# Kernel optimization log

Measured on AMD Instinct MI355X. Metric: run time of the kernel, lower is better.

The kernel has to match this reference:

```python
import jax, jax.numpy as jnp
import numpy as np

B, S, D = 2, 2048, 1024
H, DC = 16, 16          # num_heads, head_coord_dim
CD = 16                 # coord_dim
DH = D // H             # head_dim = 64


def setup_inputs() -> dict:
    key = jax.random.key(0)
    ks = jax.random.split(key, 8)
    s = 0.02
    return {
        "hidden_states": jax.random.normal(ks[0], (B, S, D), jnp.float32),
        "coordinates": jax.random.normal(ks[1], (B, S, CD), jnp.float32),
        "Wv": jax.random.normal(ks[2], (D, D), jnp.float32) * s,
        "bv": jnp.zeros((D,), jnp.float32),
        "Wc": jax.random.normal(ks[3], (H * DC, CD), jnp.float32) * s,
        "bc": jnp.zeros((H * DC,), jnp.float32),
        "Wn": jax.random.normal(ks[4], (CD, D), jnp.float32) * s,
        "bn": jnp.zeros((CD,), jnp.float32),
        "Wo": jax.random.normal(ks[5], (D, D), jnp.float32) * s,
        "bo": jnp.zeros((D,), jnp.float32),
        "gamma": jnp.zeros((1, H, 1, 1), jnp.float32),
    }


def reference(hidden_states, coordinates, Wv, bv, Wc, bc, Wn, bn, Wo, bo, gamma):
    # value: [B,S,D] -> [B,H,S,DH]
    value = (hidden_states @ Wv.T + bv).reshape(B, S, H, DH).transpose(0, 2, 1, 3)
    # coordinate heads: [B,S,CD] -> [B,H,S,DC]
    z = (coordinates @ Wc.T + bc).reshape(B, S, H, DC).transpose(0, 2, 1, 3)
    z_sq = jnp.sum(z * z, axis=-1, keepdims=True)           # [B,H,S,1]
    # pairwise squared distances [B,H,S,S]
    sq_dist = z_sq + jnp.swapaxes(z_sq, -1, -2) - 2.0 * jnp.einsum("bhsc,bhtc->bhst", z, z)
    sq_dist = jnp.maximum(sq_dist, 0.0)
    g = jax.nn.softplus(gamma)                               # [1,H,1,1]
    attn = jax.nn.softmax(-g * sq_dist, axis=-1)             # [B,H,S,S]
    out = jnp.einsum("bhst,bhtd->bhsd", attn, value)         # [B,H,S,DH]
    out = out.transpose(0, 2, 1, 3).reshape(B, S, D)
    updated_hidden = out @ Wo.T + bo
    updated_coords = hidden_states @ Wn.T + bn               # [B,S,CD]
    return updated_hidden, updated_coords
```

## Files before the change

kernel.cpp:

```cpp
#include <hip/hip_runtime.h>
#include <math.h>

typedef short short8 __attribute__((ext_vector_type(8)));
typedef short short4t __attribute__((ext_vector_type(4)));
typedef float f32x4  __attribute__((ext_vector_type(4)));

#define AS1 __attribute__((address_space(1)))
#define AS3 __attribute__((address_space(3)))

__device__ __forceinline__ unsigned cvt_pk_bf16(float lo, float hi) {
    unsigned r;
    asm("v_cvt_pk_bf16_f32 %0, %1, %2" : "=v"(r) : "v"(lo), "v"(hi));
    return r;
}
__device__ __forceinline__ unsigned f2bf_rne(float x) {
    unsigned u = __float_as_uint(x);
    return (u + 0x7fffu + ((u >> 16) & 1u)) >> 16;
}
__device__ __forceinline__ float exp2_fast(float x) {
    float r;
    asm("v_exp_f32 %0, %1" : "=v"(r) : "v"(x));
    return r;
}
__device__ __forceinline__ f32x4 mfma_k16(short4t a, short4t b, f32x4 c) {
#if __has_builtin(__builtin_amdgcn_mfma_f32_16x16x16bf16_1k)
    return __builtin_amdgcn_mfma_f32_16x16x16bf16_1k(a, b, c, 0, 0, 0);
#else
    asm volatile("v_mfma_f32_16x16x16_bf16 %0, %1, %2, %0" : "+v"(c) : "v"(a), "v"(b));
    return c;
#endif
}

__global__ __launch_bounds__(256) void prep_all(const float* __restrict__ hidden,
                                                const float* __restrict__ Wv,
                                                const float* __restrict__ Wo,
                                                const float* __restrict__ Wn,
                                                const float* __restrict__ coords,
                                                const float* __restrict__ Wc,
                                                const float* __restrict__ bc,
                                                const float* __restrict__ gamma,
                                                short* __restrict__ hsb,
                                                short* __restrict__ Wvb,
                                                short* __restrict__ Wob,
                                                short* __restrict__ Wnb,
                                                short* __restrict__ ZA,
                                                short* __restrict__ ZB) {
    __shared__ float csh[16];
    if (blockIdx.x < 3080) {
        const int i = blockIdx.x * 256 + threadIdx.x;
        const float* src;
        short* dst;
        int ii;
        if (i < 524288)      { src = hidden; dst = hsb; ii = i; }
        else if (i < 655360) { src = Wv; dst = Wvb; ii = i - 524288; }
        else if (i < 786432) { src = Wo; dst = Wob; ii = i - 655360; }
        else                 { src = Wn; dst = Wnb; ii = i - 786432; }
        const float4 a = ((const float4*)src)[2 * ii];
        const float4 b = ((const float4*)src)[2 * ii + 1];
        uint4 r;
        r.x = cvt_pk_bf16(a.x, a.y);
        r.y = cvt_pk_bf16(a.z, a.w);
        r.z = cvt_pk_bf16(b.x, b.y);
        r.w = cvt_pk_bf16(b.z, b.w);
        ((uint4*)dst)[ii] = r;
        return;
    }
    const int bs = blockIdx.x - 3080;
    const int b = bs >> 11, s = bs & 2047;
    const int tid = threadIdx.x;
    if (tid < 16) csh[tid] = coords[(size_t)bs * 16 + tid];
    __syncthreads();
    float z = bc[tid];
#pragma unroll
    for (int k = 0; k < 16; k++) z = fmaf(csh[k], Wc[tid * 16 + k], z);
    const unsigned ub = f2bf_rne(z);
    const float zb = __uint_as_float(ub << 16);
    float sq = zb * zb;
    sq += __shfl_xor(sq, 1, 64);
    sq += __shfl_xor(sq, 2, 64);
    sq += __shfl_xor(sq, 4, 64);
    sq += __shfl_xor(sq, 8, 64);
    const int h = tid >> 4, c = tid & 15;
    const float gm = gamma[h];
    const float sp = fmaxf(gm, 0.f) + log1pf(__expf(-fabsf(gm)));
    const float ch = -sp * 1.4426950408889634f;
    const size_t row = ((size_t)(b * 16 + h) * 2048 + s) * 32;
    ZA[row + c] = (short)ub;
    ZA[row + 16 + c] = (c == 0) ? (short)f2bf_rne(sq)
                                : (c == 1 ? (short)0x3F80 : (short)0);
    ZB[row + c] = (short)f2bf_rne(-2.f * ch * zb);
    ZB[row + 16 + c] = (c == 0) ? (short)f2bf_rne(ch)
                                : (c == 1 ? (short)f2bf_rne(ch * sq) : (short)0);
}

template <int EPI>
__global__ __launch_bounds__(256) void gemm_mfma(const short* __restrict__ A,
                                                 const short* __restrict__ W,
                                                 const float* __restrict__ bias,
                                                 void* __restrict__ Cout,
                                                 const short* __restrict__ Wnb,
                                                 const float* __restrict__ bn,
                                                 float* __restrict__ out1) {
    __shared__ short As[2][128][64];
    __shared__ short Bs[2][64][64];
    const int tid = threadIdx.x;
    const int wv = tid >> 6, l = tid & 63, g = l >> 4, qc = l & 15;

    if (EPI == 0 && blockIdx.x >= 512) {
        float* red = (float*)&As[0][0][0];
        const int m0 = (blockIdx.x - 512) * 16;
        const int k0 = wv * 256;
        f32x4 acc = {};
#pragma unroll
        for (int kk = 0; kk < 256; kk += 32) {
            const short8 af = *(const short8*)(A + (size_t)(m0 + qc) * 1024 + k0 + kk + g * 8);
            const short8 bf = *(const short8*)(Wnb + (size_t)qc * 1024 + k0 + kk + g * 8);
            acc = __builtin_amdgcn_mfma_f32_16x16x32_bf16(af, bf, acc, 0, 0, 0);
        }
#pragma unroll
        for (int i2 = 0; i2 < 4; i2++) red[(wv * 256) + (g * 4 + i2) * 16 + qc] = acc[i2];
        __syncthreads();
        const int r = tid >> 4, c = tid & 15;
        const float s = red[r * 16 + c] + red[256 + r * 16 + c] +
                        red[512 + r * 16 + c] + red[768 + r * 16 + c] + bn[c];
        out1[(size_t)(m0 + r) * 16 + c] = s;
        return;
    }

    const int wm = wv >> 1, wn = wv & 1;
    const int lin = blockIdx.x;
    const int wid = (lin & 7) * 64 + (lin >> 3);
    const int Mb = (wid & 31) * 128, Nb = (wid >> 5) * 64;

    auto stage = [&](int buf, int k0) {
#pragma unroll
        for (int i = 0; i < 4; i++) {
            const int c = i * 256 + tid;
            const int r = c >> 3, jp = c & 7;
            const int js = jp ^ (r & 7);
            const short* gsA = A + (size_t)(Mb + r) * 1024 + k0 + js * 8;
            short* ldsA = &As[buf][0][0] + (size_t)(i * 256 + wv * 64) * 8;
            __builtin_amdgcn_global_load_lds((const AS1 void*)gsA, (AS3 void*)ldsA, 16, 0, 0);
        }
#pragma unroll
        for (int i = 0; i < 2; i++) {
            const int c = i * 256 + tid;
            const int r = c >> 3, jp = c & 7;
            const int js = jp ^ (r & 7);
            const short* gsB = W + (size_t)(Nb + r) * 1024 + k0 + js * 8;
            short* ldsB = &Bs[buf][0][0] + (size_t)(i * 256 + wv * 64) * 8;
            __builtin_amdgcn_global_load_lds((const AS1 void*)gsB, (AS3 void*)ldsB, 16, 0, 0);
        }
    };

    f32x4 acc[4][2] = {};
    stage(0, 0);
    __syncthreads();
    int cur = 0;
#pragma unroll 1
    for (int kb = 0; kb < 16; kb++) {
        if (kb < 15) stage(cur ^ 1, (kb + 1) * 64);
#pragma unroll
        for (int ks = 0; ks < 2; ks++) {
            const int cs = ((ks * 4 + g) ^ (qc & 7)) * 8;
            short8 af[4], bfr[2];
#pragma unroll
            for (int mt = 0; mt < 4; mt++)
                af[mt] = *(const short8*)&As[cur][wm * 64 + mt * 16 + qc][cs];
#pragma unroll
            for (int nt = 0; nt < 2; nt++)
                bfr[nt] = *(const short8*)&Bs[cur][wn * 32 + nt * 16 + qc][cs];
#pragma unroll
            for (int mt = 0; mt < 4; mt++)
#pragma unroll
                for (int nt = 0; nt < 2; nt++)
                    acc[mt][nt] = __builtin_amdgcn_mfma_f32_16x16x32_bf16(af[mt], bfr[nt], acc[mt][nt], 0, 0, 0);
        }
        __syncthreads();
        cur ^= 1;
    }

    float bl[2];
#pragma unroll
    for (int nt = 0; nt < 2; nt++) bl[nt] = bias[Nb + wn * 32 + nt * 16 + qc];
#pragma unroll
    for (int mt = 0; mt < 4; mt++) {
#pragma unroll
        for (int nt = 0; nt < 2; nt++) {
            const int m0 = Mb + wm * 64 + mt * 16 + g * 4;
            const int n  = Nb + wn * 32 + nt * 16 + qc;
            f32x4 v = acc[mt][nt];
            v = v + bl[nt];
            if (EPI == 0) {
                const int bb = m0 >> 11, s0 = m0 & 2047;
                const int hh = n >> 6, dh = n & 63;
                const int s0x = s0 ^ (((n >> 3) & 1) << 2);
                uint2 p2;
                p2.x = cvt_pk_bf16(v[0], v[1]);
                p2.y = cvt_pk_bf16(v[2], v[3]);
                *(uint2*)((short*)Cout + (size_t)((bb * 16 + hh) * 64 + dh) * 2048 + s0x) = p2;
            } else {
                float* C = (float*)Cout;
#pragma unroll
                for (int i = 0; i < 4; i++) C[(size_t)(m0 + i) * 1024 + n] = v[i];
            }
        }
    }
}

__global__ __launch_bounds__(512, 4) void attn_mfma14(const short* __restrict__ ZAg,
                                                      const short* __restrict__ ZBg,
                                                      const short* __restrict__ Vt,
                                                      short* __restrict__ AOb) {
    __shared__ short Vs[2][4096];
    __shared__ short Zs[4][2048];
    const int tid = threadIdx.x;
    const int wv = tid >> 6, ln = tid & 63, g = ln >> 4, qc = ln & 15;
    const int lin = blockIdx.x;
    const int work = (lin & 7) * 64 + (lin >> 3);
    const int qb = work & 15, h = (work >> 4) & 15, b = work >> 8;
    const int bh = b * 16 + h;
    const int q0 = qb * 128 + wv * 16;

    const short* ZAb = ZAg + (size_t)bh * (2048 * 32);
    const short* ZBb = ZBg + (size_t)bh * (2048 * 32);
    const short* Vb  = Vt  + (size_t)bh * (64 * 2048);

    const short8 zq = *(const short8*)(ZBb + (size_t)(q0 + qc) * 32 + g * 8);

    union { unsigned u[2]; short4t s4; } ones4;
    ones4.u[0] = ones4.u[1] = (qc == 0) ? 0x3F803F80u : 0u;

    f32x4 acc[4] = {};
    f32x4 accl = {};

    const short* gvb = Vb + (size_t)(tid & 63) * 2048 + (tid >> 6) * 8;
    short* lvd = &Vs[0][0] + (size_t)tid * 8;
    short* lzd = &Zs[0][0] + (size_t)tid * 8;
    const int z_kt = tid >> 6, z_g = (tid >> 4) & 3, z_r = tid & 15;

    auto stageV = [&](int buf, int kb) {
        __builtin_amdgcn_global_load_lds((const AS1 void*)(gvb + kb),
                                         (AS3 void*)(lvd + buf * 4096), 16, 0, 0);
    };
    auto stageZ = [&](int buf, int kb) {
        if (tid < 256) {
            const short* gz = ZAb + (size_t)(kb + z_kt * 16 + z_r) * 32 + z_g * 8;
            __builtin_amdgcn_global_load_lds((const AS1 void*)gz,
                                             (AS3 void*)(lzd + buf * 2048), 16, 0, 0);
        }
    };

    const int vrd = (((g >> 1) * 64 + qc) * 8) + (((g & 1) ^ ((qc >> 3) & 1)) << 2);
    const int zrd = g * 128 + qc * 8;

    auto computeP = [&](int zbuf, unsigned pko[4][2]) {
        const short* Zc = &Zs[0][0] + zbuf * 2048;
        short8 zk[4];
#pragma unroll
        for (int kt = 0; kt < 4; kt++)
            zk[kt] = *(const short8*)(Zc + zrd + kt * 512);
        const f32x4 z4 = {0.f, 0.f, 0.f, 0.f};
#pragma unroll
        for (int kt = 0; kt < 4; kt++) {
            const f32x4 S = __builtin_amdgcn_mfma_f32_16x16x32_bf16(zk[kt], zq, z4, 0, 0, 0);
            pko[kt][0] = cvt_pk_bf16(exp2_fast(fminf(S[0], 0.f)), exp2_fast(fminf(S[1], 0.f)));
            pko[kt][1] = cvt_pk_bf16(exp2_fast(fminf(S[2], 0.f)), exp2_fast(fminf(S[3], 0.f)));
        }
    };
    auto doPV = [&](int buf, unsigned pkk[4][2]) {
        const short* Vc = &Vs[buf][0];
        __builtin_amdgcn_s_setprio(1);
#pragma unroll
        for (int kt = 0; kt < 4; kt++) {
            union { unsigned u[2]; short4t s4; } pb;
            pb.u[0] = pkk[kt][0];
            pb.u[1] = pkk[kt][1];
            accl = mfma_k16(ones4.s4, pb.s4, accl);
#pragma unroll
            for (int mt = 0; mt < 4; mt++)
                acc[mt] = mfma_k16(*(const short4t*)(Vc + vrd + kt * 1024 + mt * 128),
                                   pb.s4, acc[mt]);
        }
        __builtin_amdgcn_s_setprio(0);
    };

    stageV(0, 0);
    stageZ(0, 0);
    stageZ(1, 64);
    __syncthreads();

    unsigned pkA[4][2], pkB[4][2];
    computeP(0, pkA);

    int cur = 0;
#pragma unroll 1
    for (int i = 0; i < 32; i += 2) {
        if (i < 31) stageV(cur ^ 1, (i + 1) * 64);
        if (i < 30) stageZ((i + 2) & 3, (i + 2) * 64);
        computeP((i + 1) & 3, pkB);
        doPV(cur, pkA);
        __syncthreads();
        cur ^= 1;
        if (i + 1 < 31) stageV(cur ^ 1, (i + 2) * 64);
        if (i + 1 < 30) stageZ((i + 3) & 3, (i + 3) * 64);
        computeP((i + 2) & 3, pkA);
        doPV(cur, pkB);
        __syncthreads();
        cur ^= 1;
    }

    const float lv2 = __shfl(accl[0], qc, 64);
    const float inv = 1.f / lv2;
    const size_t row = (size_t)(b * 2048 + q0 + qc) * 1024 + h * 64;
#pragma unroll
    for (int mt = 0; mt < 4; mt++) {
        uint2 o;
        o.x = cvt_pk_bf16(acc[mt][0] * inv, acc[mt][1] * inv);
        o.y = cvt_pk_bf16(acc[mt][2] * inv, acc[mt][3] * inv);
        *(uint2*)(AOb + row + mt * 16 + g * 4) = o;
    }
}

extern "C" void kernel_launch(void* const* d_in, const int* in_sizes, int n_in,
                              void* d_out, int out_size, void* d_ws, size_t ws_size,
                              hipStream_t stream) {
    (void)in_sizes; (void)n_in; (void)out_size; (void)ws_size;
    const float* hidden = (const float*)d_in[0];
    const float* coords = (const float*)d_in[1];
    const float* Wv = (const float*)d_in[2];
    const float* bv = (const float*)d_in[3];
    const float* Wc = (const float*)d_in[4];
    const float* bc = (const float*)d_in[5];
    const float* Wn = (const float*)d_in[6];
    const float* bn = (const float*)d_in[7];
    const float* Wo = (const float*)d_in[8];
    const float* bo = (const float*)d_in[9];
    const float* gamma = (const float*)d_in[10];

    char* wsb = (char*)d_ws;
    short* hsb = (short*)(wsb);
    short* AOb = hsb;
    short* Wvb = (short*)(wsb + (8 << 20));
    short* Wob = (short*)(wsb + (10 << 20));
    short* Vt  = (short*)(wsb + (12 << 20));
    short* ZA  = (short*)(wsb + (20 << 20));
    short* ZB  = (short*)(wsb + (24 << 20));
    short* Wnb = (short*)(wsb + (28 << 20));

    float* out_hidden = (float*)d_out;
    float* out_coords = out_hidden + 4194304;

    prep_all<<<7176, 256, 0, stream>>>(hidden, Wv, Wo, Wn, coords, Wc, bc, gamma,
                                       hsb, Wvb, Wob, Wnb, ZA, ZB);
    gemm_mfma<0><<<768, 256, 0, stream>>>(hsb, Wvb, bv, (void*)Vt, Wnb, bn, out_coords);
    attn_mfma14<<<512, 512, 0, stream>>>(ZA, ZB, Vt, AOb);
    gemm_mfma<1><<<512, 256, 0, stream>>>(AOb, Wob, bo, (void*)out_hidden, Wnb, bn, out_coords);
}
```

Measured before the change: 96.83 us.

## Process two query tiles per wave in attention kernel to reuse V fragments

The attention kernel now uses 256-thread blocks with 4 waves, each handling 32 queries (two 16-row tiles) instead of 16. Each V fragment loaded from LDS is reused for both query tiles, and the Z fragments serve two score MFMAs, which halves LDS reads per unit of MFMA work. Staging is redistributed so every thread issues two V loads and one Z load. The cost is higher register pressure (doubled accumulators and P values), a lower launch-bounds occupancy target, and half as many waves per block to hide latency.

```diff
diff --git a/kernel.cpp b/kernel.cpp
--- a/kernel.cpp
+++ b/kernel.cpp
@@ -208,7 +208,7 @@
     }
 }
 
-__global__ __launch_bounds__(512, 4) void attn_mfma14(const short* __restrict__ ZAg,
+__global__ __launch_bounds__(256, 3) void attn_mfma15(const short* __restrict__ ZAg,
                                                       const short* __restrict__ ZBg,
                                                       const short* __restrict__ Vt,
                                                       short* __restrict__ AOb) {
@@ -220,41 +220,43 @@
     const int work = (lin & 7) * 64 + (lin >> 3);
     const int qb = work & 15, h = (work >> 4) & 15, b = work >> 8;
     const int bh = b * 16 + h;
-    const int q0 = qb * 128 + wv * 16;
+    const int q0 = qb * 128 + wv * 32;
 
     const short* ZAb = ZAg + (size_t)bh * (2048 * 32);
     const short* ZBb = ZBg + (size_t)bh * (2048 * 32);
     const short* Vb  = Vt  + (size_t)bh * (64 * 2048);
 
-    const short8 zq = *(const short8*)(ZBb + (size_t)(q0 + qc) * 32 + g * 8);
+    short8 zq[2];
+#pragma unroll
+    for (int qt = 0; qt < 2; qt++)
+        zq[qt] = *(const short8*)(ZBb + (size_t)(q0 + qt * 16 + qc) * 32 + g * 8);
 
     union { unsigned u[2]; short4t s4; } ones4;
     ones4.u[0] = ones4.u[1] = (qc == 0) ? 0x3F803F80u : 0u;
 
-    f32x4 acc[4] = {};
-    f32x4 accl = {};
-
-    const short* gvb = Vb + (size_t)(tid & 63) * 2048 + (tid >> 6) * 8;
+    f32x4 acc[2][4] = {};
+    f32x4 accl[2] = {};
+
+    const short* gvb = Vb + (size_t)ln * 2048 + wv * 8;
     short* lvd = &Vs[0][0] + (size_t)tid * 8;
     short* lzd = &Zs[0][0] + (size_t)tid * 8;
     const int z_kt = tid >> 6, z_g = (tid >> 4) & 3, z_r = tid & 15;
 
     auto stageV = [&](int buf, int kb) {
-        __builtin_amdgcn_global_load_lds((const AS1 void*)(gvb + kb),
-                                         (AS3 void*)(lvd + buf * 4096), 16, 0, 0);
+        const short* gv = gvb + kb;
+        short* lvb = lvd + buf * 4096;
+        __builtin_amdgcn_global_load_lds((const AS1 void*)gv, (AS3 void*)lvb, 16, 0, 0);
+        __builtin_amdgcn_global_load_lds((const AS1 void*)(gv + 32), (AS3 void*)(lvb + 2048), 16, 0, 0);
     };
     auto stageZ = [&](int buf, int kb) {
-        if (tid < 256) {
-            const short* gz = ZAb + (size_t)(kb + z_kt * 16 + z_r) * 32 + z_g * 8;
-            __builtin_amdgcn_global_load_lds((const AS1 void*)gz,
-                                             (AS3 void*)(lzd + buf * 2048), 16, 0, 0);
-        }
+        const short* gz = ZAb + (size_t)(kb + z_kt * 16 + z_r) * 32 + z_g * 8;
+        __builtin_amdgcn_global_load_lds((const AS1 void*)gz, (AS3 void*)(lzd + buf * 2048), 16, 0, 0);
     };
 
     const int vrd = (((g >> 1) * 64 + qc) * 8) + (((g & 1) ^ ((qc >> 3) & 1)) << 2);
     const int zrd = g * 128 + qc * 8;
 
-    auto computeP = [&](int zbuf, unsigned pko[4][2]) {
+    auto computeP = [&](int zbuf, unsigned pko[2][4][2]) {
         const short* Zc = &Zs[0][0] + zbuf * 2048;
         short8 zk[4];
 #pragma unroll
@@ -262,25 +264,33 @@
             zk[kt] = *(const short8*)(Zc + zrd + kt * 512);
         const f32x4 z4 = {0.f, 0.f, 0.f, 0.f};
 #pragma unroll
-        for (int kt = 0; kt < 4; kt++) {
-            const f32x4 S = __builtin_amdgcn_mfma_f32_16x16x32_bf16(zk[kt], zq, z4, 0, 0, 0);
-            pko[kt][0] = cvt_pk_bf16(exp2_fast(fminf(S[0], 0.f)), exp2_fast(fminf(S[1], 0.f)));
-            pko[kt][1] = cvt_pk_bf16(exp2_fast(fminf(S[2], 0.f)), exp2_fast(fminf(S[3], 0.f)));
-        }
-    };
-    auto doPV = [&](int buf, unsigned pkk[4][2]) {
+        for (int qt = 0; qt < 2; qt++)
+#pragma unroll
+            for (int kt = 0; kt < 4; kt++) {
+                const f32x4 S = __builtin_amdgcn_mfma_f32_16x16x32_bf16(zk[kt], zq[qt], z4, 0, 0, 0);
+                pko[qt][kt][0] = cvt_pk_bf16(exp2_fast(fminf(S[0], 0.f)), exp2_fast(fminf(S[1], 0.f)));
+                pko[qt][kt][1] = cvt_pk_bf16(exp2_fast(fminf(S[2], 0.f)), exp2_fast(fminf(S[3], 0.f)));
+            }
+    };
+    auto doPV = [&](int buf, unsigned pkk[2][4][2]) {
         const short* Vc = &Vs[buf][0];
         __builtin_amdgcn_s_setprio(1);
 #pragma unroll
         for (int kt = 0; kt < 4; kt++) {
-            union { unsigned u[2]; short4t s4; } pb;
-            pb.u[0] = pkk[kt][0];
-            pb.u[1] = pkk[kt][1];
-            accl = mfma_k16(ones4.s4, pb.s4, accl);
+            short4t vf[4];
 #pragma unroll
             for (int mt = 0; mt < 4; mt++)
-                acc[mt] = mfma_k16(*(const short4t*)(Vc + vrd + kt * 1024 + mt * 128),
-                                   pb.s4, acc[mt]);
+                vf[mt] = *(const short4t*)(Vc + vrd + kt * 1024 + mt * 128);
+#pragma unroll
+            for (int qt = 0; qt < 2; qt++) {
+                union { unsigned u[2]; short4t s4; } pb;
+                pb.u[0] = pkk[qt][kt][0];
+                pb.u[1] = pkk[qt][kt][1];
+                accl[qt] = mfma_k16(ones4.s4, pb.s4, accl[qt]);
+#pragma unroll
+                for (int mt = 0; mt < 4; mt++)
+                    acc[qt][mt] = mfma_k16(vf[mt], pb.s4, acc[qt][mt]);
+            }
         }
         __builtin_amdgcn_s_setprio(0);
     };
@@ -290,7 +300,7 @@
     stageZ(1, 64);
     __syncthreads();
 
-    unsigned pkA[4][2], pkB[4][2];
+    unsigned pkA[2][4][2], pkB[2][4][2];
     computeP(0, pkA);
 
     int cur = 0;
@@ -310,15 +320,18 @@
         cur ^= 1;
     }
 
-    const float lv2 = __shfl(accl[0], qc, 64);
-    const float inv = 1.f / lv2;
-    const size_t row = (size_t)(b * 2048 + q0 + qc) * 1024 + h * 64;
-#pragma unroll
-    for (int mt = 0; mt < 4; mt++) {
-        uint2 o;
-        o.x = cvt_pk_bf16(acc[mt][0] * inv, acc[mt][1] * inv);
-        o.y = cvt_pk_bf16(acc[mt][2] * inv, acc[mt][3] * inv);
-        *(uint2*)(AOb + row + mt * 16 + g * 4) = o;
+#pragma unroll
+    for (int qt = 0; qt < 2; qt++) {
+        const float lv2 = __shfl(accl[qt][0], qc, 64);
+        const float inv = 1.f / lv2;
+        const size_t row = (size_t)(b * 2048 + q0 + qt * 16 + qc) * 1024 + h * 64;
+#pragma unroll
+        for (int mt = 0; mt < 4; mt++) {
+            uint2 o;
+            o.x = cvt_pk_bf16(acc[qt][mt][0] * inv, acc[qt][mt][1] * inv);
+            o.y = cvt_pk_bf16(acc[qt][mt][2] * inv, acc[qt][mt][3] * inv);
+            *(uint2*)(AOb + row + mt * 16 + g * 4) = o;
+        }
     }
 }
 
@@ -354,6 +367,6 @@
     prep_all<<<7176, 256, 0, stream>>>(hidden, Wv, Wo, Wn, coords, Wc, bc, gamma,
                                        hsb, Wvb, Wob, Wnb, ZA, ZB);
     gemm_mfma<0><<<768, 256, 0, stream>>>(hsb, Wvb, bv, (void*)Vt, Wnb, bn, out_coords);
-    attn_mfma14<<<512, 512, 0, stream>>>(ZA, ZB, Vt, AOb);
+    attn_mfma15<<<512, 256, 0, stream>>>(ZA, ZB, Vt, AOb);
     gemm_mfma<1><<<512, 256, 0, stream>>>(AOb, Wob, bo, (void*)out_hidden, Wnb, bn, out_coords);
 }
```

Result: slower. 100.6 us (+3.9%).
